# Kernel tuning notes

Measured on AMD Instinct MI355X. Metric: run time of the kernel, lower is better.

Reference implementation:

```python
import jax, jax.numpy as jnp
import numpy as np

N_NODES = 50000
N_EDGES = 800000
D_FEAT = 128      # node feature dim (== coef_dim)
COEF_DIM = 128
OUT_DIM = 128     # node_layer / neighbour_layer output dim
EPS = 1e-12       # tf.math.l2_normalize epsilon


def setup_inputs() -> dict:
    key = jax.random.key(0)
    ks = jax.random.split(key, 8)
    s = 1.0 / np.sqrt(D_FEAT)
    h = jax.random.normal(ks[0], (N_NODES, D_FEAT), dtype=jnp.float32)
    src = jax.random.randint(ks[1], (N_EDGES,), 0, N_NODES, dtype=jnp.int32)
    dst = jax.random.randint(ks[2], (N_EDGES,), 0, N_NODES, dtype=jnp.int32)
    W_coef = jax.random.normal(ks[3], (D_FEAT, COEF_DIM), dtype=jnp.float32) * s
    b_coef = jnp.zeros((COEF_DIM,), dtype=jnp.float32)
    W_red = jax.random.normal(ks[4], (2 * COEF_DIM, 1), dtype=jnp.float32) * (1.0 / np.sqrt(2 * COEF_DIM))
    b_red = jnp.zeros((1,), dtype=jnp.float32)
    W_node = jax.random.normal(ks[5], (D_FEAT, OUT_DIM), dtype=jnp.float32) * s
    b_node = jnp.zeros((OUT_DIM,), dtype=jnp.float32)
    W_neigh = jax.random.normal(ks[6], (D_FEAT, OUT_DIM), dtype=jnp.float32) * s
    b_neigh = jnp.zeros((OUT_DIM,), dtype=jnp.float32)
    return {"h": h, "src": src, "dst": dst,
            "W_coef": W_coef, "b_coef": b_coef,
            "W_red": W_red, "b_red": b_red,
            "W_node": W_node, "b_node": b_node,
            "W_neigh": W_neigh, "b_neigh": b_neigh}


def reference(h, src, dst, W_coef, b_coef, W_red, b_red, W_node, b_node, W_neigh, b_neigh):
    n = h.shape[0]
    # message func: per-edge coef transform of source features (activation=None)
    q = h @ W_coef + b_coef                      # [N, C] dst-side coef features
    m = q[src]                                   # [E, C] (coef_layer(h[src]))
    # reduce func: attention score per edge from concat(dst coef, message)
    e = jnp.concatenate([q[dst], m], axis=-1) @ W_red + b_red   # [E, 1]
    e = e[:, 0]
    # softmax over incoming edges of each destination node (stable)
    emax = jax.ops.segment_max(e, dst, num_segments=n)          # [N]
    ex = jnp.exp(e - emax[dst])                                 # [E]
    denom = jax.ops.segment_sum(ex, dst, num_segments=n)        # [N]
    alpha = ex / (denom[dst] + EPS)                             # [E]
    # weighted neighbour aggregation of raw source features ('neigh' mailbox)
    agg = jax.ops.segment_sum(alpha[:, None] * h[src], dst, num_segments=n)  # [N, D]
    # new_h = concat(node_layer(h), neighbour_layer(agg))
    new_h = jnp.concatenate([h @ W_node + b_node, agg @ W_neigh + b_neigh], axis=-1)  # [N, 2*OUT]
    # tf.math.l2_normalize along last axis
    sq = jnp.sum(new_h * new_h, axis=-1, keepdims=True)
    return new_h * jax.lax.rsqrt(jnp.maximum(sq, EPS))
```

## Files before the change

kernel.cpp:

```cpp
#include <hip/hip_runtime.h>
#include <hip/hip_bf16.h>
#include <math.h>

#define N_NODES 50000
#define N_EDGES 800000
#define D_FEAT  128
#define EPSF    1e-12f

#define NPG     120
#define NG      417
#define CHUNK_E 4096
#define NCHUNK  196
#define GCAP    2560

#define OFF_U2      0
#define OFF_GCUR    1024
#define OFF_S       4096
#define OFF_ROWPTR  204800
#define OFF_WTN     405504
#define OFF_WTG     438272
#define OFF_SSRCW   471040
#define OFF_HB      6871040
#define OFF_BUCKET  19671040

typedef __attribute__((ext_vector_type(8))) short bf8;
typedef __attribute__((ext_vector_type(4))) float f4;

__global__ void make_u2_kernel(const float* __restrict__ W_coef,
                               const float* __restrict__ W_red,
                               float* __restrict__ u2, int* __restrict__ gcursor) {
    __shared__ float wr[128];
    int k = threadIdx.x;
    wr[k] = W_red[128 + k];
    for (int i = k; i < NG; i += 128) gcursor[i] = 0;
    __syncthreads();
    const float4* row = (const float4*)(W_coef + k * 128);
    float acc = 0.f;
    #pragma unroll
    for (int j = 0; j < 32; ++j) {
        float4 v = row[j];
        acc += v.x * wr[4*j] + v.y * wr[4*j+1] + v.z * wr[4*j+2] + v.w * wr[4*j+3];
    }
    u2[k] = acc;
}

__global__ __launch_bounds__(256) void prep_kernel(
        const float* __restrict__ h, const float* __restrict__ u2,
        const float* __restrict__ Wn, const float* __restrict__ Wg,
        const int* __restrict__ src, const int* __restrict__ dst,
        float* __restrict__ s, unsigned short* __restrict__ hb,
        unsigned short* __restrict__ WtN, unsigned short* __restrict__ WtG,
        int* __restrict__ gcursor, int* __restrict__ bucket) {
    int b = blockIdx.x;
    if (b < 12500) {
        int node = b * 4 + (threadIdx.x >> 6);
        int lane = threadIdx.x & 63;
        float2 hv = ((const float2*)(h + (size_t)node * 128))[lane];
        float2 uv = ((const float2*)u2)[lane];
        float v = hv.x * uv.x + hv.y * uv.y;
        #pragma unroll
        for (int off = 32; off; off >>= 1) v += __shfl_xor(v, off);
        if (lane == 0) s[node] = v;
        __hip_bfloat162 p = __float22bfloat162_rn(hv);
        ((unsigned int*)(hb + (size_t)node * 128))[lane] = *(unsigned int*)&p;
    } else if (b < 12564) {
        int idx = (b - 12500) * 256 + threadIdx.x;
        int n = idx >> 7, k = idx & 127;
        __hip_bfloat16 a = __float2bfloat16(Wn[k * 128 + n]);
        __hip_bfloat16 g = __float2bfloat16(Wg[k * 128 + n]);
        WtN[n * 128 + k] = *(unsigned short*)&a;
        WtG[n * 128 + k] = *(unsigned short*)&g;
    } else {
        __shared__ int lh[NG];
        __shared__ int base[NG];
        __shared__ int cnt2[NG];
        int chunk = b - 12564;
        int tid = threadIdx.x;
        for (int i = tid; i < NG; i += 256) { lh[i] = 0; cnt2[i] = 0; }
        __syncthreads();
        int base_e = chunk * CHUNK_E;
        #pragma unroll
        for (int it = 0; it < CHUNK_E / 256; ++it) {
            int e = base_e + it * 256 + tid;
            if (e < N_EDGES) atomicAdd(&lh[(unsigned)dst[e] / NPG], 1);
        }
        __syncthreads();
        for (int i = tid; i < NG; i += 256) {
            int c = lh[i];
            base[i] = c ? atomicAdd(&gcursor[i], c) : 0;
        }
        __syncthreads();
        #pragma unroll
        for (int it = 0; it < CHUNK_E / 256; ++it) {
            int e = base_e + it * 256 + tid;
            if (e < N_EDGES) {
                int d = dst[e];
                int g = (unsigned)d / NPG;
                int r = atomicAdd(&cnt2[g], 1);
                int p = base[g] + r;
                if (p < GCAP)
                    bucket[(size_t)g * GCAP + p] = src[e] | ((d - g * NPG) << 16);
            }
        }
    }
}

__global__ __launch_bounds__(128) void fine_kernel(
        const int* __restrict__ gcnt, const int* __restrict__ bucket,
        const float* __restrict__ s,
        int* __restrict__ row_ptr, int2* __restrict__ ssrc_w) {
    __shared__ int cnt[NPG];
    __shared__ int cnt2[NPG];
    __shared__ int sexcl[NPG];
    __shared__ int ws[2];
    __shared__ int red[2];
    int g = blockIdx.x, tid = threadIdx.x;
    int lane = tid & 63, wid = tid >> 6;

    int partial = 0;
    for (int i = tid; i < g; i += 128) partial += gcnt[i];
    #pragma unroll
    for (int off = 32; off; off >>= 1) partial += __shfl_down(partial, off);
    if (lane == 0) red[wid] = partial;
    if (tid < NPG) { cnt[tid] = 0; cnt2[tid] = 0; }
    __syncthreads();
    int beg = red[0] + red[1];
    int cnt_g = min(gcnt[g], GCAP);
    const int* bk = bucket + (size_t)g * GCAP;

    for (int i = tid; i < cnt_g; i += 128)
        atomicAdd(&cnt[bk[i] >> 16], 1);
    __syncthreads();
    int v = (tid < NPG) ? cnt[tid] : 0;
    int incl = v;
    #pragma unroll
    for (int off = 1; off < 64; off <<= 1) {
        int t = __shfl_up(incl, off);
        if (lane >= off) incl += t;
    }
    if (lane == 63) ws[wid] = incl;
    __syncthreads();
    if (wid == 1) incl += ws[0];
    int excl = incl - v;
    if (tid < NPG) sexcl[tid] = excl;
    int node = g * NPG + tid;
    if (tid < NPG && node < N_NODES) row_ptr[node] = beg + excl;
    if (g == NG - 1 && tid == 0) row_ptr[N_NODES] = N_EDGES;
    __syncthreads();
    for (int i = tid; i < cnt_g; i += 128) {
        int p = bk[i];
        int loc = p >> 16;
        int sv = p & 0xFFFF;
        float wv = __expf(s[sv]);
        int r = atomicAdd(&cnt2[loc], 1);
        ssrc_w[beg + sexcl[loc] + r] = make_int2(sv, __float_as_int(wv));
    }
}

__global__ __launch_bounds__(1024) void agg_gemm_kernel(
        const int* __restrict__ row_ptr, const int2* __restrict__ ssrc_w,
        const unsigned short* __restrict__ hb,
        const unsigned short* __restrict__ WtN, const unsigned short* __restrict__ WtG,
        const float* __restrict__ b_node, const float* __restrict__ b_neigh,
        float* __restrict__ out) {
    __shared__ __align__(16) unsigned short aggt[16][136];
    __shared__ float ssrp[16][16];
    int wave = threadIdx.x >> 6, lane = threadIdx.x & 63;
    int node0 = blockIdx.x * 16;
    int q = lane >> 4, l16 = lane & 15;

    {
        int node = node0 + wave;
        int beg = row_ptr[node];
        int deg = row_ptr[node + 1] - beg;
        float acc[8] = {0.f, 0.f, 0.f, 0.f, 0.f, 0.f, 0.f, 0.f};
        float wsum = 0.f;
        int ngroups = (deg + 3) >> 2;
        #pragma unroll 2
        for (int j = 0; j < ngroups; ++j) {
            int e4 = 4 * j + q;
            int ec = min(e4, deg - 1);
            int2 pw = ssrc_w[beg + ec];
            float wv = (e4 < deg) ? __int_as_float(pw.y) : 0.f;
            wsum += wv;
            uint4 hv = *(const uint4*)(hb + (size_t)pw.x * 128 + l16 * 8);
            acc[0] = fmaf(wv, __uint_as_float(hv.x << 16),        acc[0]);
            acc[1] = fmaf(wv, __uint_as_float(hv.x & 0xFFFF0000u), acc[1]);
            acc[2] = fmaf(wv, __uint_as_float(hv.y << 16),        acc[2]);
            acc[3] = fmaf(wv, __uint_as_float(hv.y & 0xFFFF0000u), acc[3]);
            acc[4] = fmaf(wv, __uint_as_float(hv.z << 16),        acc[4]);
            acc[5] = fmaf(wv, __uint_as_float(hv.z & 0xFFFF0000u), acc[5]);
            acc[6] = fmaf(wv, __uint_as_float(hv.w << 16),        acc[6]);
            acc[7] = fmaf(wv, __uint_as_float(hv.w & 0xFFFF0000u), acc[7]);
        }
        #pragma unroll
        for (int i = 0; i < 8; ++i) {
            acc[i] += __shfl_xor(acc[i], 16);
            acc[i] += __shfl_xor(acc[i], 32);
        }
        wsum += __shfl_xor(wsum, 16);
        wsum += __shfl_xor(wsum, 32);
        float inv = 1.f / (wsum + EPSF);
        if (q == 0) {
            unsigned o[4];
            #pragma unroll
            for (int j2 = 0; j2 < 4; ++j2) {
                __hip_bfloat162 p = __float22bfloat162_rn(
                    make_float2(acc[2*j2] * inv, acc[2*j2+1] * inv));
                o[j2] = *(unsigned*)&p;
            }
            *(uint4*)&aggt[wave][l16 * 8] = make_uint4(o[0], o[1], o[2], o[3]);
        }
    }
    __syncthreads();

    int t = wave & 7, half = wave >> 3;
    const unsigned short* Wt = half ? WtG : WtN;
    f4 acc = (f4){0.f, 0.f, 0.f, 0.f};
    #pragma unroll
    for (int kc = 0; kc < 4; ++kc) {
        int kbase = kc * 32 + q * 8;
        bf8 a = half ? *(const bf8*)&aggt[l16][kbase]
                     : *(const bf8*)(hb + (size_t)(node0 + l16) * 128 + kbase);
        bf8 bb = *(const bf8*)(Wt + (size_t)(t * 16 + l16) * 128 + kbase);
        acc = __builtin_amdgcn_mfma_f32_16x16x32_bf16(a, bb, acc, 0, 0, 0);
    }

    float bv = (half ? b_neigh : b_node)[t * 16 + l16];
    float ssr[4];
    #pragma unroll
    for (int r = 0; r < 4; ++r) {
        acc[r] += bv;
        ssr[r] = acc[r] * acc[r];
    }
    #pragma unroll
    for (int r = 0; r < 4; ++r) {
        ssr[r] += __shfl_xor(ssr[r], 1);
        ssr[r] += __shfl_xor(ssr[r], 2);
        ssr[r] += __shfl_xor(ssr[r], 4);
        ssr[r] += __shfl_xor(ssr[r], 8);
    }
    if (l16 == 0) {
        #pragma unroll
        for (int r = 0; r < 4; ++r) ssrp[wave][q * 4 + r] = ssr[r];
    }
    __syncthreads();
    #pragma unroll
    for (int r = 0; r < 4; ++r) {
        int row = q * 4 + r;
        float tot = 0.f;
        #pragma unroll
        for (int w2 = 0; w2 < 16; ++w2) tot += ssrp[w2][row];
        float sc = rsqrtf(fmaxf(tot, EPSF));
        size_t node = node0 + row;
        out[node * 256 + half * 128 + t * 16 + l16] = acc[r] * sc;
    }
}

extern "C" void kernel_launch(void* const* d_in, const int* in_sizes, int n_in,
                              void* d_out, int out_size, void* d_ws, size_t ws_size,
                              hipStream_t stream) {
    const float* h       = (const float*)d_in[0];
    const int*   src     = (const int*)d_in[1];
    const int*   dst     = (const int*)d_in[2];
    const float* W_coef  = (const float*)d_in[3];
    const float* W_red   = (const float*)d_in[5];
    const float* W_node  = (const float*)d_in[7];
    const float* b_node  = (const float*)d_in[8];
    const float* W_neigh = (const float*)d_in[9];
    const float* b_neigh = (const float*)d_in[10];
    float* out = (float*)d_out;

    char* w = (char*)d_ws;
    float*          u2      = (float*)(w + OFF_U2);
    int*            gcursor = (int*)(w + OFF_GCUR);
    float*          s       = (float*)(w + OFF_S);
    int*            row_ptr = (int*)(w + OFF_ROWPTR);
    unsigned short* WtN     = (unsigned short*)(w + OFF_WTN);
    unsigned short* WtG     = (unsigned short*)(w + OFF_WTG);
    int2*           ssrc_w  = (int2*)(w + OFF_SSRCW);
    unsigned short* hb      = (unsigned short*)(w + OFF_HB);
    int*            bucket  = (int*)(w + OFF_BUCKET);

    make_u2_kernel<<<1, 128, 0, stream>>>(W_coef, W_red, u2, gcursor);
    prep_kernel<<<12500 + 64 + NCHUNK, 256, 0, stream>>>(
        h, u2, W_node, W_neigh, src, dst, s, hb, WtN, WtG, gcursor, bucket);
    fine_kernel<<<NG, 128, 0, stream>>>(gcursor, bucket, s, row_ptr, ssrc_w);
    agg_gemm_kernel<<<N_NODES / 16, 1024, 0, stream>>>(
        row_ptr, ssrc_w, hb, WtN, WtG, b_node, b_neigh, out);
}
```

Measured before the change: 223.6 us.

## Restructure aggregation to 16 lanes per node and 4 MFMA tiles per wave

The aggregation phase now gives each destination node 16 lanes that walk its edge list serially, so the cross-lane shuffle reduction and the padding of the last edge group are gone. The block covers 32 nodes with 512 threads, and each wave reuses one A fragment across four B tiles in the MFMA stage, so the normalization reduction only has to sum four partials. The exponential of the per-node score moves to prep, computed once per node instead of once per edge. Serial per-node loops may lengthen the critical path on high-degree nodes and reduce memory-level parallelism per node.

New measurement: 198.6 us. 1.13x faster.

```diff
diff --git a/kernel.cpp b/kernel.cpp
--- a/kernel.cpp
+++ b/kernel.cpp
@@ -15,7 +15,7 @@
 
 #define OFF_U2      0
 #define OFF_GCUR    1024
-#define OFF_S       4096
+#define OFF_ES      4096
 #define OFF_ROWPTR  204800
 #define OFF_WTN     405504
 #define OFF_WTG     438272
@@ -48,7 +48,7 @@
         const float* __restrict__ h, const float* __restrict__ u2,
         const float* __restrict__ Wn, const float* __restrict__ Wg,
         const int* __restrict__ src, const int* __restrict__ dst,
-        float* __restrict__ s, unsigned short* __restrict__ hb,
+        float* __restrict__ es, unsigned short* __restrict__ hb,
         unsigned short* __restrict__ WtN, unsigned short* __restrict__ WtG,
         int* __restrict__ gcursor, int* __restrict__ bucket) {
     int b = blockIdx.x;
@@ -60,7 +60,7 @@
         float v = hv.x * uv.x + hv.y * uv.y;
         #pragma unroll
         for (int off = 32; off; off >>= 1) v += __shfl_xor(v, off);
-        if (lane == 0) s[node] = v;
+        if (lane == 0) es[node] = __expf(v);
         __hip_bfloat162 p = __float22bfloat162_rn(hv);
         ((unsigned int*)(hb + (size_t)node * 128))[lane] = *(unsigned int*)&p;
     } else if (b < 12564) {
@@ -107,7 +107,7 @@
 
 __global__ __launch_bounds__(128) void fine_kernel(
         const int* __restrict__ gcnt, const int* __restrict__ bucket,
-        const float* __restrict__ s,
+        const float* __restrict__ es,
         int* __restrict__ row_ptr, int2* __restrict__ ssrc_w) {
     __shared__ int cnt[NPG];
     __shared__ int cnt2[NPG];
@@ -151,37 +151,39 @@
         int p = bk[i];
         int loc = p >> 16;
         int sv = p & 0xFFFF;
-        float wv = __expf(s[sv]);
+        float wv = es[sv];
         int r = atomicAdd(&cnt2[loc], 1);
         ssrc_w[beg + sexcl[loc] + r] = make_int2(sv, __float_as_int(wv));
     }
 }
 
-__global__ __launch_bounds__(1024) void agg_gemm_kernel(
+__global__ __launch_bounds__(512) void agg_gemm_kernel(
         const int* __restrict__ row_ptr, const int2* __restrict__ ssrc_w,
         const unsigned short* __restrict__ hb,
         const unsigned short* __restrict__ WtN, const unsigned short* __restrict__ WtG,
         const float* __restrict__ b_node, const float* __restrict__ b_neigh,
         float* __restrict__ out) {
-    __shared__ __align__(16) unsigned short aggt[16][136];
-    __shared__ float ssrp[16][16];
-    int wave = threadIdx.x >> 6, lane = threadIdx.x & 63;
-    int node0 = blockIdx.x * 16;
+    __shared__ __align__(16) unsigned short aggt[32][136];
+    __shared__ float ssrp[8][16];
+    int tid = threadIdx.x;
+    int wave = tid >> 6, lane = tid & 63;
+    int node0 = blockIdx.x * 32;
     int q = lane >> 4, l16 = lane & 15;
 
     {
-        int node = node0 + wave;
-        int beg = row_ptr[node];
-        int deg = row_ptr[node + 1] - beg;
+        int g32 = tid >> 4;
+        int node = node0 + g32;
+        int beg = 0, deg = 0;
+        if (node < N_NODES) {
+            beg = row_ptr[node];
+            deg = row_ptr[node + 1] - beg;
+        }
         float acc[8] = {0.f, 0.f, 0.f, 0.f, 0.f, 0.f, 0.f, 0.f};
         float wsum = 0.f;
-        int ngroups = (deg + 3) >> 2;
-        #pragma unroll 2
-        for (int j = 0; j < ngroups; ++j) {
-            int e4 = 4 * j + q;
-            int ec = min(e4, deg - 1);
-            int2 pw = ssrc_w[beg + ec];
-            float wv = (e4 < deg) ? __int_as_float(pw.y) : 0.f;
+        #pragma unroll 4
+        for (int i = 0; i < deg; ++i) {
+            int2 pw = ssrc_w[beg + i];
+            float wv = __int_as_float(pw.y);
             wsum += wv;
             uint4 hv = *(const uint4*)(hb + (size_t)pw.x * 128 + l16 * 8);
             acc[0] = fmaf(wv, __uint_as_float(hv.x << 16),        acc[0]);
@@ -193,45 +195,49 @@
             acc[6] = fmaf(wv, __uint_as_float(hv.w << 16),        acc[6]);
             acc[7] = fmaf(wv, __uint_as_float(hv.w & 0xFFFF0000u), acc[7]);
         }
-        #pragma unroll
-        for (int i = 0; i < 8; ++i) {
-            acc[i] += __shfl_xor(acc[i], 16);
-            acc[i] += __shfl_xor(acc[i], 32);
-        }
-        wsum += __shfl_xor(wsum, 16);
-        wsum += __shfl_xor(wsum, 32);
         float inv = 1.f / (wsum + EPSF);
-        if (q == 0) {
-            unsigned o[4];
-            #pragma unroll
-            for (int j2 = 0; j2 < 4; ++j2) {
-                __hip_bfloat162 p = __float22bfloat162_rn(
-                    make_float2(acc[2*j2] * inv, acc[2*j2+1] * inv));
-                o[j2] = *(unsigned*)&p;
-            }
-            *(uint4*)&aggt[wave][l16 * 8] = make_uint4(o[0], o[1], o[2], o[3]);
-        }
-    }
-    __syncthreads();
-
-    int t = wave & 7, half = wave >> 3;
+        unsigned o[4];
+        #pragma unroll
+        for (int j = 0; j < 4; ++j) {
+            __hip_bfloat162 p = __float22bfloat162_rn(
+                make_float2(acc[2*j] * inv, acc[2*j+1] * inv));
+            o[j] = *(unsigned*)&p;
+        }
+        *(uint4*)&aggt[g32][l16 * 8] = make_uint4(o[0], o[1], o[2], o[3]);
+    }
+    __syncthreads();
+
+    int rt = wave & 1, tq = wave >> 1;
+    int half = tq >> 1, tb = (tq & 1) * 4;
     const unsigned short* Wt = half ? WtG : WtN;
-    f4 acc = (f4){0.f, 0.f, 0.f, 0.f};
+    size_t arow = (size_t)min(node0 + rt * 16 + l16, N_NODES - 1);
+
+    f4 acc[4];
+    #pragma unroll
+    for (int tt = 0; tt < 4; ++tt) acc[tt] = (f4){0.f, 0.f, 0.f, 0.f};
     #pragma unroll
     for (int kc = 0; kc < 4; ++kc) {
         int kbase = kc * 32 + q * 8;
-        bf8 a = half ? *(const bf8*)&aggt[l16][kbase]
-                     : *(const bf8*)(hb + (size_t)(node0 + l16) * 128 + kbase);
-        bf8 bb = *(const bf8*)(Wt + (size_t)(t * 16 + l16) * 128 + kbase);
-        acc = __builtin_amdgcn_mfma_f32_16x16x32_bf16(a, bb, acc, 0, 0, 0);
-    }
-
-    float bv = (half ? b_neigh : b_node)[t * 16 + l16];
-    float ssr[4];
-    #pragma unroll
-    for (int r = 0; r < 4; ++r) {
-        acc[r] += bv;
-        ssr[r] = acc[r] * acc[r];
+        bf8 a = half ? *(const bf8*)&aggt[rt * 16 + l16][kbase]
+                     : *(const bf8*)(hb + arow * 128 + kbase);
+        #pragma unroll
+        for (int tt = 0; tt < 4; ++tt) {
+            int t = tb + tt;
+            bf8 bb = *(const bf8*)(Wt + (size_t)(t * 16 + l16) * 128 + kbase);
+            acc[tt] = __builtin_amdgcn_mfma_f32_16x16x32_bf16(a, bb, acc[tt], 0, 0, 0);
+        }
+    }
+
+    float ssr[4] = {0.f, 0.f, 0.f, 0.f};
+    #pragma unroll
+    for (int tt = 0; tt < 4; ++tt) {
+        int t = tb + tt;
+        float bv = (half ? b_neigh : b_node)[t * 16 + l16];
+        #pragma unroll
+        for (int r = 0; r < 4; ++r) {
+            acc[tt][r] += bv;
+            ssr[r] = fmaf(acc[tt][r], acc[tt][r], ssr[r]);
+        }
     }
     #pragma unroll
     for (int r = 0; r < 4; ++r) {
@@ -248,12 +254,16 @@
     #pragma unroll
     for (int r = 0; r < 4; ++r) {
         int row = q * 4 + r;
-        float tot = 0.f;
-        #pragma unroll
-        for (int w2 = 0; w2 < 16; ++w2) tot += ssrp[w2][row];
+        float tot = ssrp[rt][row] + ssrp[rt + 2][row] +
+                    ssrp[rt + 4][row] + ssrp[rt + 6][row];
         float sc = rsqrtf(fmaxf(tot, EPSF));
-        size_t node = node0 + row;
-        out[node * 256 + half * 128 + t * 16 + l16] = acc[r] * sc;
+        int node = node0 + rt * 16 + row;
+        if (node < N_NODES) {
+            float* o = out + (size_t)node * 256 + half * 128;
+            #pragma unroll
+            for (int tt = 0; tt < 4; ++tt)
+                o[(tb + tt) * 16 + l16] = acc[tt][r] * sc;
+        }
     }
 }
 
@@ -274,7 +284,7 @@
     char* w = (char*)d_ws;
     float*          u2      = (float*)(w + OFF_U2);
     int*            gcursor = (int*)(w + OFF_GCUR);
-    float*          s       = (float*)(w + OFF_S);
+    float*          es      = (float*)(w + OFF_ES);
     int*            row_ptr = (int*)(w + OFF_ROWPTR);
     unsigned short* WtN     = (unsigned short*)(w + OFF_WTN);
     unsigned short* WtG     = (unsigned short*)(w + OFF_WTG);
@@ -284,8 +294,8 @@
 
     make_u2_kernel<<<1, 128, 0, stream>>>(W_coef, W_red, u2, gcursor);
     prep_kernel<<<12500 + 64 + NCHUNK, 256, 0, stream>>>(
-        h, u2, W_node, W_neigh, src, dst, s, hb, WtN, WtG, gcursor, bucket);
-    fine_kernel<<<NG, 128, 0, stream>>>(gcursor, bucket, s, row_ptr, ssrc_w);
-    agg_gemm_kernel<<<N_NODES / 16, 1024, 0, stream>>>(
+        h, u2, W_node, W_neigh, src, dst, es, hb, WtN, WtG, gcursor, bucket);
+    fine_kernel<<<NG, 128, 0, stream>>>(gcursor, bucket, es, row_ptr, ssrc_w);
+    agg_gemm_kernel<<<(N_NODES + 31) / 32, 512, 0, stream>>>(
         row_ptr, ssrc_w, hb, WtN, WtG, b_node, b_neigh, out);
 }
```
